# Optimization experiments

Hardware: AMD Instinct MI355X
Metric: run time of the kernel (lower is better)

## Reference

```python
import jax, jax.numpy as jnp
import numpy as np

H = 8  # num_heads
NEG = -1000000.0

def _ln(x, g, b):
    m = jnp.mean(x, axis=-1, keepdims=True)
    v = jnp.var(x, axis=-1, keepdims=True)
    return (x - m) / jnp.sqrt(v + 1e-5) * g + b


def setup_inputs() -> dict:
    key = jax.random.key(0)
    ks = jax.random.split(key, 24)
    B, T, D = 8, 1024, 1024
    Lt, Nt, K, Rt, E = 768, 77, 2, 512, 2048
    s = 0.02
    r = lambda i, shape: s * jax.random.normal(ks[i], shape, jnp.float32)
    return {
        "x": jax.random.normal(ks[0], (B, T, D), jnp.float32),
        "xf": jax.random.normal(ks[1], (B, Nt, Lt), jnp.float32),
        "emb": jax.random.normal(ks[2], (B, E), jnp.float32),
        "src_mask": jnp.ones((B, T, 1), jnp.float32),
        "cond_type": jax.random.randint(ks[3], (B, 1, 1), 0, 100),
        "re_motion": jax.random.normal(ks[4], (B, K, Rt, D), jnp.float32),
        "re_text": jax.random.normal(ks[5], (B, K, 1, D), jnp.float32),
        "re_mask": jnp.ones((B, K, Rt), jnp.float32),
        "ln_g": jnp.ones((D,)), "ln_b": jnp.zeros((D,)),
        "tln_g": jnp.ones((Lt,)), "tln_b": jnp.zeros((Lt,)),
        "rn1_g": jnp.ones((2 * D,)), "rn1_b": jnp.zeros((2 * D,)),
        "rn2_g": jnp.ones((D,)), "rn2_b": jnp.zeros((D,)),
        "Wq": r(6, (D, D)), "bq": jnp.zeros((D,)),
        "Wkt": r(7, (Lt, D)), "bkt": jnp.zeros((D,)),
        "Wvt": r(8, (Lt, D)), "bvt": jnp.zeros((D,)),
        "Wkm": r(9, (D, D)), "bkm": jnp.zeros((D,)),
        "Wvm": r(10, (D, D)), "bvm": jnp.zeros((D,)),
        "Wkr": r(11, (2 * D, D)), "bkr": jnp.zeros((D,)),
        "Wvr": r(12, (D, D)), "bvr": jnp.zeros((D,)),  # zero-init in original; random here for nontrivial math
        "We": r(13, (E, 2 * D)), "be": jnp.zeros((2 * D,)),
        "sln_g": jnp.ones((D,)), "sln_b": jnp.zeros((D,)),
        "Wo": r(14, (D, D)), "bo": jnp.zeros((D,)),  # zero-init in original
    }


def reference(x, xf, emb, src_mask, cond_type, re_motion, re_text, re_mask,
              ln_g, ln_b, tln_g, tln_b, rn1_g, rn1_b, rn2_g, rn2_b,
              Wq, bq, Wkt, bkt, Wvt, bvt, Wkm, bkm, Wvm, bvm,
              Wkr, bkr, Wvr, bvr, We, be, sln_g, sln_b, Wo, bo):
    B, T, D = x.shape
    K, Rt = re_motion.shape[1], re_motion.shape[2]

    norm_x = _ln(x, ln_g, ln_b)
    norm_xf = _ln(xf, tln_g, tln_b)
    query = norm_x @ Wq + bq  # (B,T,D)

    text_ct = (cond_type % 10 > 0).astype(x.dtype)   # (B,1,1)
    retr_ct = (cond_type // 10 > 0).astype(x.dtype)  # (B,1,1)
    re_mask_r = re_mask.reshape(B, -1, 1)            # (B,K*Rt,1)

    # retrieval key features: concat(motion, repeated text) along channels
    re_text_rep = jnp.broadcast_to(re_text, (B, K, Rt, D))
    re_feat_key = jnp.concatenate([re_motion, re_text_rep], axis=-1).reshape(B, -1, 2 * D)

    key_text = norm_xf @ Wkt + bkt + (1.0 - text_ct) * NEG
    key_retr = _ln(re_feat_key, rn1_g, rn1_b) @ Wkr + bkr \
        + (1.0 - retr_ct) * NEG + (1.0 - re_mask_r) * NEG
    key_motion = norm_x @ Wkm + bkm + (1.0 - src_mask) * NEG
    key = jnp.concatenate([key_text, key_retr, key_motion], axis=1)  # (B,N,D)
    N = key.shape[1]

    q = jax.nn.softmax(query.reshape(B, T, H, -1), axis=-1)  # softmax over head dim
    k = jax.nn.softmax(key.reshape(B, N, H, -1), axis=1)     # softmax over tokens

    value_text = (norm_xf @ Wvt + bvt) * text_ct
    value_retr = (_ln(re_motion.reshape(B, -1, D), rn2_g, rn2_b) @ Wvr + bvr) * retr_ct * re_mask_r
    value_motion = (norm_x @ Wvm + bvm) * src_mask
    v = jnp.concatenate([value_text, value_retr, value_motion], axis=1).reshape(B, N, H, -1)

    att = jnp.einsum('bnhd,bnhl->bhdl', k, v)          # (B,H,dh,dh)
    y = jnp.einsum('bthd,bhdl->bthl', q, att).reshape(B, T, D)

    # StylizationBlock: FiLM from time embedding, then zero-init out proj (eval: dropout = id)
    eo = jax.nn.silu(emb) @ We + be                    # (B,2D)
    scale, shift = jnp.split(eo[:, None, :], 2, axis=2)
    h = _ln(y, sln_g, sln_b) * (1.0 + scale) + shift
    h = jax.nn.silu(h) @ Wo + bo
    return x + h
```

## Files before the change

### kernel.cpp

```cpp
#include <hip/hip_runtime.h>
#include <hip/hip_bf16.h>
#include <math.h>

using bf16 = __hip_bfloat16;

typedef short s16x8 __attribute__((ext_vector_type(8)));
typedef short s16x4 __attribute__((ext_vector_type(4)));
typedef float f32x4 __attribute__((ext_vector_type(4)));

constexpr int Bc = 8, Tc = 1024, Dc = 1024, Hc = 8;
constexpr int NTc = 77, LTc = 768, KRc = 1024, Nc = 2125, Ec = 2048;
constexpr float NEGC = -1000000.0f;

constexpr int NP = 2128;
constexpr long SKT = (long)Dc * NP;

constexpr long F_STATS1 = 0;
constexpr long F_STATS2 = F_STATS1 + 16384;
constexpr long F_KEYADD = F_STATS2 + 16384;
constexpr long F_VALMUL = F_KEYADD + 17000;
constexpr long F_SILU   = F_VALMUL + 17000;
constexpr long F_EO     = F_SILU + 16384;
constexpr long F_ATT    = F_EO + 16384;
constexpr long F_END    = F_ATT + 1048576;
constexpr long KT_SZ   = (long)Bc * Dc * NP;
constexpr long B_NORMX = 0;
constexpr long B_Q     = B_NORMX + 8388608;
constexpr long B_KT    = B_Q + 8388608;
constexpr long B_VT    = B_KT + KT_SZ;
constexpr long B_NXF   = B_VT + KT_SZ;
constexpr long B_WQ    = B_NXF + 473088;
constexpr long B_WKM   = B_WQ + 1048576;
constexpr long B_WVM   = B_WKM + 1048576;
constexpr long B_WKT   = B_WVM + 1048576;
constexpr long B_WVT   = B_WKT + 786432;
constexpr long B_WKR   = B_WVT + 786432;
constexpr long B_WVR   = B_WKR + 2097152;
constexpr long B_WO    = B_WVR + 1048576;
constexpr long B_END   = B_WO + 1048576;
constexpr long B_REN2  = B_END;
constexpr long REN2_SZ = 8388608;
constexpr size_t WS_NEED = (size_t)F_END * 4 + (size_t)B_END * 2;
constexpr size_t WS_BIG  = (size_t)F_END * 4 + (size_t)(B_END + REN2_SZ) * 2;

__device__ __forceinline__ float b2f(bf16 v) { return __bfloat162float(v); }
__device__ __forceinline__ bf16 f2b(float v) { return __float2bfloat16(v); }
__device__ __forceinline__ short f2s(float v) {
    bf16 h = __float2bfloat16(v);
    return *reinterpret_cast<short*>(&h);
}
__device__ __forceinline__ float us2f(unsigned short u) {
    bf16 h = *reinterpret_cast<bf16*>(&u);
    return __bfloat162float(h);
}
__device__ __forceinline__ void storef(float* p, float v) { *p = v; }
__device__ __forceinline__ void storef(bf16* p, float v) { *p = __float2bfloat16(v); }

typedef __attribute__((address_space(1))) const unsigned int gu32;
typedef __attribute__((address_space(3))) unsigned int lu32;
__device__ __forceinline__ void gl_lds16(const void* g, void* l) {
    __builtin_amdgcn_global_load_lds((gu32*)g, (lu32*)l, 16, 0, 0);
}

__device__ __forceinline__ float2 block_sum2(float s, float s2) {
    #pragma unroll
    for (int off = 32; off > 0; off >>= 1) {
        s  += __shfl_down(s, off, 64);
        s2 += __shfl_down(s2, off, 64);
    }
    __shared__ float sh[4], sh2[4];
    int w = threadIdx.x >> 6, lane = threadIdx.x & 63;
    if (lane == 0) { sh[w] = s; sh2[w] = s2; }
    __syncthreads();
    s = sh[0] + sh[1] + sh[2] + sh[3];
    s2 = sh2[0] + sh2[1] + sh2[2] + sh2[3];
    return make_float2(s, s2);
}

__device__ __forceinline__ void ln_row_dev(const float* __restrict__ x,
                                           const float* __restrict__ g,
                                           const float* __restrict__ b,
                                           bf16* __restrict__ o, int C) {
    float s = 0.f, s2 = 0.f;
    for (int c = threadIdx.x; c < C; c += 256) { float v = x[c]; s += v; s2 += v * v; }
    float2 r = block_sum2(s, s2);
    float mean = r.x / C;
    float var = r.y / C - mean * mean;
    float inv = rsqrtf(var + 1e-5f);
    for (int c = threadIdx.x; c < C; c += 256)
        o[c] = f2b((x[c] - mean) * inv * g[c] + b[c]);
}

__device__ __forceinline__ s16x4 pack4(float4 v, float mean, float rstd, float4 g, float4 b) {
    s16x4 o;
    o[0] = f2s((v.x - mean) * rstd * g.x + b.x);
    o[1] = f2s((v.y - mean) * rstd * g.y + b.y);
    o[2] = f2s((v.z - mean) * rstd * g.z + b.z);
    o[3] = f2s((v.w - mean) * rstd * g.w + b.w);
    return o;
}

__global__ __launch_bounds__(256) void fused_pre(
    const float* __restrict__ x, const float* __restrict__ ln_g,
    const float* __restrict__ ln_b, bf16* __restrict__ norm_x,
    const float* __restrict__ xf, const float* __restrict__ tln_g,
    const float* __restrict__ tln_b, bf16* __restrict__ nxf,
    const float* __restrict__ motion, const float* __restrict__ text,
    const float* __restrict__ g1, const float* __restrict__ b1,
    const float* __restrict__ g2, const float* __restrict__ b2,
    bf16* __restrict__ ren1, bf16* __restrict__ ren2,
    const int* __restrict__ cond_type, const float* __restrict__ src_mask,
    const float* __restrict__ re_mask,
    float* __restrict__ key_add, float* __restrict__ val_mul,
    bf16* __restrict__ vT) {
    int bid = blockIdx.x;
    if (bid < 8192) {
        long row = bid;
        ln_row_dev(x + row * 1024, ln_g, ln_b, norm_x + row * 1024, 1024);
    } else if (bid < 8808) {
        long row = bid - 8192;
        ln_row_dev(xf + row * 768, tln_g, tln_b, nxf + row * 768, 768);
    } else if (bid < 17000) {
        long row = bid - 8808;
        int c = threadIdx.x * 4;
        const float* mrow = motion + row * 1024;
        const float* trow = text + (row >> 9) * 1024;
        float4 mv = *(const float4*)(mrow + c);
        float4 tv = *(const float4*)(trow + c);
        float sm = mv.x + mv.y + mv.z + mv.w;
        float sm2 = mv.x * mv.x + mv.y * mv.y + mv.z * mv.z + mv.w * mv.w;
        float2 rm = block_sum2(sm, sm2);
        __syncthreads();
        float st = tv.x + tv.y + tv.z + tv.w;
        float st2 = tv.x * tv.x + tv.y * tv.y + tv.z * tv.z + tv.w * tv.w;
        float2 rt = block_sum2(st, st2);
        float mean2 = rm.x / 1024.f;
        float var2 = rm.y / 1024.f - mean2 * mean2;
        float r2 = rsqrtf(var2 + 1e-5f);
        float mean1 = (rm.x + rt.x) / 2048.f;
        float var1 = (rm.y + rt.y) / 2048.f - mean1 * mean1;
        float r1 = rsqrtf(var1 + 1e-5f);
        float4 g1m = *(const float4*)(g1 + c),        b1m = *(const float4*)(b1 + c);
        float4 g1t = *(const float4*)(g1 + 1024 + c), b1t = *(const float4*)(b1 + 1024 + c);
        float4 g2m = *(const float4*)(g2 + c),        b2m = *(const float4*)(b2 + c);
        *(s16x4*)((short*)ren1 + row * 2048 + c)        = pack4(mv, mean1, r1, g1m, b1m);
        *(s16x4*)((short*)ren1 + row * 2048 + 1024 + c) = pack4(tv, mean1, r1, g1t, b1t);
        *(s16x4*)((short*)ren2 + row * 1024 + c)        = pack4(mv, mean2, r2, g2m, b2m);
    } else {
        int b2i = bid - 17000;
        if (b2i < 67) {
            int idx = b2i * 256 + threadIdx.x;
            if (idx >= Bc * Nc) return;
            int b = idx / Nc, n = idx % Nc;
            int ct = cond_type[b];
            float text_ct = ((ct % 10) > 0) ? 1.f : 0.f;
            float retr_ct = ((ct / 10) > 0) ? 1.f : 0.f;
            float add, mul;
            if (n < NTc) {
                add = (1.f - text_ct) * NEGC; mul = text_ct;
            } else if (n < NTc + KRc) {
                float rm = re_mask[b * KRc + (n - NTc)];
                add = (1.f - retr_ct) * NEGC + (1.f - rm) * NEGC;
                mul = retr_ct * rm;
            } else {
                float sm = src_mask[b * Tc + (n - NTc - KRc)];
                add = (1.f - sm) * NEGC; mul = sm;
            }
            key_add[idx] = add;
            val_mul[idx] = mul;
        } else {
            int row = (b2i - 67) * 256 + threadIdx.x;
            if (row >= Bc * Dc) return;
            bf16* p = vT + (long)row * NP + Nc;
            p[0] = f2b(0.f); p[1] = f2b(0.f); p[2] = f2b(0.f);
        }
    }
}

__global__ __launch_bounds__(256) void fused_w(
    const float* __restrict__ Wq,  const float* __restrict__ Wkt,
    const float* __restrict__ Wvt, const float* __restrict__ Wkm,
    const float* __restrict__ Wvm, const float* __restrict__ Wkr,
    const float* __restrict__ Wvr, const float* __restrict__ Wo,
    short* __restrict__ WtQ,  short* __restrict__ WtKT,
    short* __restrict__ WtVT, short* __restrict__ WtKM,
    short* __restrict__ WtVM, short* __restrict__ WtKR,
    short* __restrict__ WtVR, short* __restrict__ WtO,
    const float* __restrict__ emb, const float* __restrict__ We,
    float* __restrict__ part) {
    __shared__ float t[32][33];
    int bid = blockIdx.x;
    if (bid < 8704) {
        int sy = bid >> 5;
        int n0 = (bid & 31) * 32;
        const float* W; short* Wt; int K; int ky;
        if (sy < 32)       { W = Wq;  Wt = WtQ;  K = 1024; ky = sy; }
        else if (sy < 56)  { W = Wkt; Wt = WtKT; K = 768;  ky = sy - 32; }
        else if (sy < 80)  { W = Wvt; Wt = WtVT; K = 768;  ky = sy - 56; }
        else if (sy < 112) { W = Wkm; Wt = WtKM; K = 1024; ky = sy - 80; }
        else if (sy < 144) { W = Wvm; Wt = WtVM; K = 1024; ky = sy - 112; }
        else if (sy < 208) { W = Wkr; Wt = WtKR; K = 2048; ky = sy - 144; }
        else if (sy < 240) { W = Wvr; Wt = WtVR; K = 1024; ky = sy - 208; }
        else               { W = Wo;  Wt = WtO;  K = 1024; ky = sy - 240; }
        int k0 = ky * 32;
        int tx = threadIdx.x & 31, ty = threadIdx.x >> 5;
        #pragma unroll
        for (int i = 0; i < 4; ++i)
            t[ty + i * 8][tx] = W[(long)(k0 + ty + i * 8) * 1024 + n0 + tx];
        __syncthreads();
        #pragma unroll
        for (int i = 0; i < 4; ++i)
            Wt[(long)(n0 + ty + i * 8) * K + k0 + tx] = f2s(t[tx][ty + i * 8]);
    } else {
        int l = bid - 8704;
        int nb = l & 7, ks = l >> 3;
        int n = nb * 256 + threadIdx.x;
        int k0 = ks * 64;
        __shared__ float a_s[8][64];
        for (int idx = threadIdx.x; idx < 512; idx += 256) {
            int b = idx >> 6, kk = idx & 63;
            float v = emb[b * 2048 + k0 + kk];
            a_s[b][kk] = v / (1.f + expf(-v));
        }
        __syncthreads();
        float acc[8] = {};
        for (int kk = 0; kk < 64; ++kk) {
            float w = We[(long)(k0 + kk) * 2048 + n];
            #pragma unroll
            for (int b = 0; b < 8; ++b) acc[b] = fmaf(a_s[b][kk], w, acc[b]);
        }
        #pragma unroll
        for (int b = 0; b < 8; ++b) part[((long)ks * 8 + b) * 2048 + n] = acc[b];
    }
}

constexpr int LDK = 64;

__global__ __launch_bounds__(256) void gemm_mega(
    const short* __restrict__ norm_x, const short* __restrict__ ren1,
    const short* __restrict__ ren2, const short* __restrict__ nxf,
    const short* __restrict__ WtQKVM, const short* __restrict__ WtKR,
    const short* __restrict__ WtVR, const short* __restrict__ WtTXT,
    const float* __restrict__ bq, const float* __restrict__ bkm,
    const float* __restrict__ bvm, const float* __restrict__ bkr,
    const float* __restrict__ bvr,
    const float* __restrict__ bkt, const float* __restrict__ bvt,
    const float* __restrict__ key_add, const float* __restrict__ val_mul,
    bf16* __restrict__ q16, bf16* __restrict__ kT, bf16* __restrict__ vT) {
    int jid = blockIdx.x;
    int sect, tm, tn, K, M, lda, bb = 0;
    const short* A; const short* Bt;
    if (jid < 512) {
        sect = 0;
        int s = (jid & 7) * 64 + (jid >> 3);
        bb = s >> 6; int r = s & 63;
        tm = (r >> 3) * 128; tn = (r & 7) * 128;
        A = ren1 + (long)bb * KRc * 2048; lda = 2048; K = 2048; M = 1024;
        Bt = WtKR;
    } else if (jid < 2048) {
        sect = 1;
        int l = jid - 512;
        int s = (l & 7) * 192 + (l >> 3);
        tn = (s % 24) * 128; tm = (s / 24) * 128;
        A = norm_x; lda = 1024; K = 1024; M = 8192;
        Bt = WtQKVM;
    } else if (jid < 2176) {
        sect = 2;
        int l = jid - 2048;
        bb = l >> 4; tn = (l & 15) * 128; tm = 0;
        A = nxf + (long)bb * NTc * LTc; lda = 768; K = 768; M = 77;
        Bt = WtTXT;
    } else {
        sect = 3;
        int l = jid - 2176;
        int s = (l & 7) * 64 + (l >> 3);
        bb = s >> 6; int r = s & 63;
        tm = (r >> 3) * 128; tn = (r & 7) * 128;
        A = ren2 + (long)bb * KRc * 1024; lda = 1024; K = 1024; M = 1024;
        Bt = WtVR;
    }
    const int ldb = lda;
    const bool swap_ops = !(sect == 1 && tn < 1024);

    __shared__ __align__(16) short As[128 * LDK];
    __shared__ __align__(16) short Bs[128 * LDK];

    int tid = threadIdx.x;
    int lane = tid & 63, wid = tid >> 6;
    int wi = wid >> 1, wj = wid & 1;
    int l16 = lane & 15, quad = lane >> 4;

    f32x4 acc[4][4];
    #pragma unroll
    for (int i = 0; i < 4; ++i)
        #pragma unroll
        for (int j = 0; j < 4; ++j)
            acc[i][j] = (f32x4){0.f, 0.f, 0.f, 0.f};

    auto issue = [&](int k0) {
        #pragma unroll
        for (int p = 0; p < 4; ++p) {
            int e = p * 256 + tid;
            int row = e >> 3, c8 = e & 7;
            int gm = tm + row;
            if (gm >= M) gm = M - 1;
            gl_lds16(A + (long)gm * lda + k0 + c8 * 8, &As[row * LDK + c8 * 8]);
            gl_lds16(Bt + (long)(tn + row) * ldb + k0 + c8 * 8, &Bs[row * LDK + c8 * 8]);
        }
    };

    issue(0);
    int kt = 0;
    while (true) {
        __syncthreads();
        #pragma unroll
        for (int kk = 0; kk < 2; ++kk) {
            s16x8 af[4], bfr[4];
            #pragma unroll
            for (int i = 0; i < 4; ++i)
                af[i] = *(const s16x8*)&As[(wi * 64 + i * 16 + l16) * LDK + kk * 32 + quad * 8];
            #pragma unroll
            for (int j = 0; j < 4; ++j)
                bfr[j] = *(const s16x8*)&Bs[(wj * 64 + j * 16 + l16) * LDK + kk * 32 + quad * 8];
            if (swap_ops) {
                #pragma unroll
                for (int i = 0; i < 4; ++i)
                    #pragma unroll
                    for (int j = 0; j < 4; ++j)
                        acc[i][j] = __builtin_amdgcn_mfma_f32_16x16x32_bf16(bfr[j], af[i], acc[i][j], 0, 0, 0);
            } else {
                #pragma unroll
                for (int i = 0; i < 4; ++i)
                    #pragma unroll
                    for (int j = 0; j < 4; ++j)
                        acc[i][j] = __builtin_amdgcn_mfma_f32_16x16x32_bf16(af[i], bfr[j], acc[i][j], 0, 0, 0);
            }
        }
        int nxt = kt + 64;
        if (nxt >= K) break;
        __syncthreads();
        issue(nxt);
        kt = nxt;
    }

    if (sect == 1 && tn < 1024) {
        #pragma unroll
        for (int i = 0; i < 4; ++i) {
            #pragma unroll
            for (int r = 0; r < 4; ++r) {
                int gm = tm + wi * 64 + i * 16 + quad * 4 + r;
                #pragma unroll
                for (int j = 0; j < 4; ++j) {
                    int gn = tn + wj * 64 + j * 16 + l16;
                    q16[(long)gm * Dc + gn] = f2b(acc[i][j][r] + bq[gn]);
                }
            }
        }
    } else if (sect == 1) {
        int sec = tn >> 10, fn0 = tn & 1023;
        const float* bias = (sec == 1) ? bkm : bvm;
        bf16* C = (sec == 1) ? kT : vT;
        #pragma unroll
        for (int j = 0; j < 4; ++j) {
            #pragma unroll
            for (int r = 0; r < 4; ++r) {
                int feat = fn0 + wj * 64 + j * 16 + quad * 4 + r;
                float bf_ = bias[feat];
                #pragma unroll
                for (int i = 0; i < 4; ++i) {
                    int gm = tm + wi * 64 + i * 16 + l16;
                    int b = gm >> 10, tok = gm & 1023;
                    int mi = b * Nc + NTc + KRc + tok;
                    float v = acc[i][j][r] + bf_;
                    if (sec == 1) v += key_add[mi];
                    else          v *= val_mul[mi];
                    C[(long)b * SKT + (long)feat * NP + NTc + KRc + tok] = f2b(v);
                }
            }
        }
    } else if (sect == 0) {
        const float* rmask = key_add + bb * Nc + NTc;
        bf16* C = kT + (long)bb * SKT + NTc;
        #pragma unroll
        for (int j = 0; j < 4; ++j) {
            #pragma unroll
            for (int r = 0; r < 4; ++r) {
                int feat = tn + wj * 64 + j * 16 + quad * 4 + r;
                float bf_ = bkr[feat];
                #pragma unroll
                for (int i = 0; i < 4; ++i) {
                    int tok = tm + wi * 64 + i * 16 + l16;
                    C[(long)feat * NP + tok] = f2b(acc[i][j][r] + bf_ + rmask[tok]);
                }
            }
        }
    } else if (sect == 3) {
        const float* rmask = val_mul + bb * Nc + NTc;
        bf16* C = vT + (long)bb * SKT + NTc;
        #pragma unroll
        for (int j = 0; j < 4; ++j) {
            #pragma unroll
            for (int r = 0; r < 4; ++r) {
                int feat = tn + wj * 64 + j * 16 + quad * 4 + r;
                float bf_ = bvr[feat];
                #pragma unroll
                for (int i = 0; i < 4; ++i) {
                    int tok = tm + wi * 64 + i * 16 + l16;
                    C[(long)feat * NP + tok] = f2b((acc[i][j][r] + bf_) * rmask[tok]);
                }
            }
        }
    } else {
        int sec = tn >> 10, fn0 = tn & 1023;
        const float* bias = sec ? bvt : bkt;
        const float* rmask = (sec ? val_mul : key_add) + bb * Nc;
        bf16* C = (sec ? vT : kT) + (long)bb * SKT;
        #pragma unroll
        for (int j = 0; j < 4; ++j) {
            #pragma unroll
            for (int r = 0; r < 4; ++r) {
                int feat = fn0 + wj * 64 + j * 16 + quad * 4 + r;
                float bf_ = bias[feat];
                #pragma unroll
                for (int i = 0; i < 4; ++i) {
                    int tok = wi * 64 + i * 16 + l16;
                    if (tok >= NTc) continue;
                    float v = acc[i][j][r] + bf_;
                    if (sec) v *= rmask[tok];
                    else     v += rmask[tok];
                    C[(long)feat * NP + tok] = f2b(v);
                }
            }
        }
    }
}

__global__ __launch_bounds__(256) void gemm_vr(
    const short* __restrict__ ren2, const short* __restrict__ WtVR,
    const float* __restrict__ bvr, const float* __restrict__ val_mul,
    bf16* __restrict__ vT) {
    int s = (blockIdx.x & 7) * 64 + (blockIdx.x >> 3);
    int b = s >> 6; int r = s & 63;
    const int tm = (r >> 3) * 128;
    const int tn = (r & 7) * 128;
    const short* A = ren2 + (long)b * KRc * 1024;
    const float* rmask = val_mul + b * Nc + NTc;
    bf16* C = vT + (long)b * SKT + NTc;

    __shared__ __align__(16) short As[128 * LDK];
    __shared__ __align__(16) short Bs[128 * LDK];

    int tid = threadIdx.x;
    int lane = tid & 63, wid = tid >> 6;
    int wi = wid >> 1, wj = wid & 1;
    int l16 = lane & 15, quad = lane >> 4;

    f32x4 acc[4][4];
    #pragma unroll
    for (int i = 0; i < 4; ++i)
        #pragma unroll
        for (int j = 0; j < 4; ++j)
            acc[i][j] = (f32x4){0.f, 0.f, 0.f, 0.f};

    auto issue = [&](int k0) {
        #pragma unroll
        for (int p = 0; p < 4; ++p) {
            int e = p * 256 + tid;
            int row = e >> 3, c8 = e & 7;
            gl_lds16(A + (long)(tm + row) * 1024 + k0 + c8 * 8, &As[row * LDK + c8 * 8]);
            gl_lds16(WtVR + (long)(tn + row) * 1024 + k0 + c8 * 8, &Bs[row * LDK + c8 * 8]);
        }
    };

    issue(0);
    int kt = 0;
    while (true) {
        __syncthreads();
        #pragma unroll
        for (int kk = 0; kk < 2; ++kk) {
            s16x8 af[4], bfr[4];
            #pragma unroll
            for (int i = 0; i < 4; ++i)
                af[i] = *(const s16x8*)&As[(wi * 64 + i * 16 + l16) * LDK + kk * 32 + quad * 8];
            #pragma unroll
            for (int j = 0; j < 4; ++j)
                bfr[j] = *(const s16x8*)&Bs[(wj * 64 + j * 16 + l16) * LDK + kk * 32 + quad * 8];
            #pragma unroll
            for (int i = 0; i < 4; ++i)
                #pragma unroll
                for (int j = 0; j < 4; ++j)
                    acc[i][j] = __builtin_amdgcn_mfma_f32_16x16x32_bf16(bfr[j], af[i], acc[i][j], 0, 0, 0);
        }
        int nxt = kt + 64;
        if (nxt >= 1024) break;
        __syncthreads();
        issue(nxt);
        kt = nxt;
    }

    #pragma unroll
    for (int j = 0; j < 4; ++j) {
        #pragma unroll
        for (int r2 = 0; r2 < 4; ++r2) {
            int feat = tn + wj * 64 + j * 16 + quad * 4 + r2;
            float bf_ = bvr[feat];
            #pragma unroll
            for (int i = 0; i < 4; ++i) {
                int tok = tm + wi * 64 + i * 16 + l16;
                C[(long)feat * NP + tok] = f2b((acc[i][j][r2] + bf_) * rmask[tok]);
            }
        }
    }
}

__global__ __launch_bounds__(256) void gemm_out(
    const short* __restrict__ A, const short* __restrict__ Bt,
    const float* __restrict__ bias, const float* __restrict__ addC,
    float* __restrict__ C) {
    int s = (blockIdx.x & 7) * 128 + (blockIdx.x >> 3);
    const int tm = (s >> 4) * 128;
    const int tn = (s & 15) * 64;

    __shared__ __align__(16) short As[128 * LDK];
    __shared__ __align__(16) short Bs[64 * LDK];

    int tid = threadIdx.x;
    int lane = tid & 63, wid = tid >> 6;
    int wi = wid >> 1, wj = wid & 1;
    int l16 = lane & 15, quad = lane >> 4;

    f32x4 acc[4][2];
    #pragma unroll
    for (int i = 0; i < 4; ++i)
        #pragma unroll
        for (int j = 0; j < 2; ++j)
            acc[i][j] = (f32x4){0.f, 0.f, 0.f, 0.f};

    auto issue = [&](int k0) {
        #pragma unroll
        for (int p = 0; p < 4; ++p) {
            int e = p * 256 + tid;
            int row = e >> 3, c8 = e & 7;
            gl_lds16(A + (long)(tm + row) * 1024 + k0 + c8 * 8, &As[row * LDK + c8 * 8]);
        }
        #pragma unroll
        for (int p = 0; p < 2; ++p) {
            int e = p * 256 + tid;
            int row = e >> 3, c8 = e & 7;
            gl_lds16(Bt + (long)(tn + row) * 1024 + k0 + c8 * 8, &Bs[row * LDK + c8 * 8]);
        }
    };

    issue(0);
    int kt = 0;
    while (true) {
        __syncthreads();
        #pragma unroll
        for (int kk = 0; kk < 2; ++kk) {
            s16x8 af[4], bfr[2];
            #pragma unroll
            for (int i = 0; i < 4; ++i)
                af[i] = *(const s16x8*)&As[(wi * 64 + i * 16 + l16) * LDK + kk * 32 + quad * 8];
            #pragma unroll
            for (int j = 0; j < 2; ++j)
                bfr[j] = *(const s16x8*)&Bs[(wj * 32 + j * 16 + l16) * LDK + kk * 32 + quad * 8];
            #pragma unroll
            for (int i = 0; i < 4; ++i)
                #pragma unroll
                for (int j = 0; j < 2; ++j)
                    acc[i][j] = __builtin_amdgcn_mfma_f32_16x16x32_bf16(af[i], bfr[j], acc[i][j], 0, 0, 0);
        }
        int nxt = kt + 64;
        if (nxt >= 1024) break;
        __syncthreads();
        issue(nxt);
        kt = nxt;
    }

    #pragma unroll
    for (int i = 0; i < 4; ++i) {
        #pragma unroll
        for (int r = 0; r < 4; ++r) {
            int gm = tm + wi * 64 + i * 16 + quad * 4 + r;
            #pragma unroll
            for (int j = 0; j < 2; ++j) {
                int gn = tn + wj * 32 + j * 16 + l16;
                C[(long)gm * 1024 + gn] = acc[i][j][r] + bias[gn] + addC[(long)gm * 1024 + gn];
            }
        }
    }
}

__global__ __launch_bounds__(256) void fused_sm(
    bf16* __restrict__ q, const bf16* __restrict__ kT,
    float* __restrict__ cs_m, float* __restrict__ cs_inv,
    const float* __restrict__ part, const float* __restrict__ be,
    float* __restrict__ eo) {
    int bid = blockIdx.x;
    int lane = threadIdx.x & 63;
    if (bid < 16384) {
        long row = (long)bid * 4 + (threadIdx.x >> 6);
        bf16* p = q + row * 128 + lane * 2;
        float v0 = b2f(p[0]), v1 = b2f(p[1]);
        float mx = fmaxf(v0, v1);
        #pragma unroll
        for (int off = 32; off > 0; off >>= 1) mx = fmaxf(mx, __shfl_xor(mx, off, 64));
        float e0 = expf(v0 - mx), e1 = expf(v1 - mx);
        float s = e0 + e1;
        #pragma unroll
        for (int off = 32; off > 0; off >>= 1) s += __shfl_xor(s, off, 64);
        float inv = 1.f / s;
        p[0] = f2b(e0 * inv);
        p[1] = f2b(e1 * inv);
    } else if (bid < 18432) {
        int row = (bid - 16384) * 4 + (threadIdx.x >> 6);
        const s16x8* p8 = (const s16x8*)(kT + (long)row * NP);
        float m = -3.0e38f;
        for (int c = lane; c < NP / 8; c += 64) {
            s16x8 raw = p8[c];
            int n0 = c * 8;
            #pragma unroll
            for (int j = 0; j < 8; ++j)
                if (n0 + j < Nc) m = fmaxf(m, us2f((unsigned short)raw[j]));
        }
        #pragma unroll
        for (int off = 32; off > 0; off >>= 1) m = fmaxf(m, __shfl_xor(m, off, 64));
        float s = 0.f;
        for (int c = lane; c < NP / 8; c += 64) {
            s16x8 raw = p8[c];
            int n0 = c * 8;
            #pragma unroll
            for (int j = 0; j < 8; ++j)
                if (n0 + j < Nc) s += __expf(us2f((unsigned short)raw[j]) - m);
        }
        #pragma unroll
        for (int off = 32; off > 0; off >>= 1) s += __shfl_xor(s, off, 64);
        if (lane == 0) { cs_m[row] = m; cs_inv[row] = 1.f / s; }
    } else {
        int idx = (bid - 18432) * 256 + threadIdx.x;
        int n = idx & 2047, b = idx >> 11;
        float s = be[n];
        #pragma unroll 8
        for (int ks = 0; ks < 32; ++ks) s += part[((long)ks * 8 + b) * 2048 + n];
        eo[idx] = s;
    }
}

constexpr int ATT_SPLIT = 8;
__global__ __launch_bounds__(256) void att_gemm(const bf16* __restrict__ kTb,
                                                const bf16* __restrict__ vTb,
                                                const float* __restrict__ cs_m,
                                                float* __restrict__ att_part) {
    int bh = blockIdx.x;
    int split = blockIdx.y;
    int b = bh >> 3, h = bh & 7;
    const short* A  = (const short*)kTb + ((long)b * 1024 + h * 128) * NP;
    const short* Bt = (const short*)vTb + ((long)b * 1024 + h * 128) * NP;
    float* ap = att_part + ((long)split * 64 + bh) * 16384;

    __shared__ __align__(16) short As[128 * LDK];
    __shared__ __align__(16) short Bs[128 * LDK];
    __shared__ float ms[128];

    int tid = threadIdx.x;
    if (tid < 128) ms[tid] = cs_m[(long)b * 1024 + h * 128 + tid];

    int lane = tid & 63, wid = tid >> 6;
    int wi = wid >> 1, wj = wid & 1;
    int l16 = lane & 15, quad = lane >> 4;

    f32x4 acc[4][4];
    #pragma unroll
    for (int i = 0; i < 4; ++i)
        #pragma unroll
        for (int j = 0; j < 4; ++j)
            acc[i][j] = (f32x4){0.f, 0.f, 0.f, 0.f};

    uint4 pa[4];
    auto computeA = [&](int k0) {
        #pragma unroll
        for (int p = 0; p < 4; ++p) {
            int e = p * 256 + tid;
            int row = e >> 3, c8 = e & 7;
            int n0 = k0 + c8 * 8;
            union { short s[8]; uint4 u; } pk;
            if (n0 >= Nc) {
                pk.u = (uint4){0u, 0u, 0u, 0u};
            } else {
                float m = ms[row];
                s16x8 raw = *(const s16x8*)(A + (long)row * NP + n0);
                #pragma unroll
                for (int j = 0; j < 8; ++j) {
                    float v = (n0 + j < Nc) ? __expf(us2f((unsigned short)raw[j]) - m) : 0.f;
                    pk.s[j] = f2s(v);
                }
            }
            pa[p] = pk.u;
        }
    };
    auto issueB = [&](int k0) {
        #pragma unroll
        for (int p = 0; p < 4; ++p) {
            int e = p * 256 + tid;
            int row = e >> 3, c8 = e & 7;
            int n0 = k0 + c8 * 8;
            if (n0 > NP - 8) n0 = NP - 8;
            gl_lds16(Bt + (long)row * NP + n0, &Bs[row * LDK + c8 * 8]);
        }
    };
    auto storeA = [&]() {
        #pragma unroll
        for (int p = 0; p < 4; ++p) {
            int e = p * 256 + tid;
            int row = e >> 3, c8 = e & 7;
            *(uint4*)&As[row * LDK + c8 * 8] = pa[p];
        }
    };

    int st = (split < 2) ? split * 5 : 10 + (split - 2) * 4;
    int cnt = (split < 2) ? 5 : 4;
    int kt = st * 64;
    int kend = kt + cnt * 64;

    __syncthreads();
    issueB(kt);
    computeA(kt);
    storeA();
    while (true) {
        __syncthreads();
        #pragma unroll
        for (int kk = 0; kk < 2; ++kk) {
            s16x8 af[4], bfr[4];
            #pragma unroll
            for (int i = 0; i < 4; ++i)
                af[i] = *(const s16x8*)&As[(wi * 64 + i * 16 + l16) * LDK + kk * 32 + quad * 8];
            #pragma unroll
            for (int j = 0; j < 4; ++j)
                bfr[j] = *(const s16x8*)&Bs[(wj * 64 + j * 16 + l16) * LDK + kk * 32 + quad * 8];
            #pragma unroll
            for (int i = 0; i < 4; ++i)
                #pragma unroll
                for (int j = 0; j < 4; ++j)
                    acc[i][j] = __builtin_amdgcn_mfma_f32_16x16x32_bf16(bfr[j], af[i], acc[i][j], 0, 0, 0);
        }
        int nxt = kt + 64;
        if (nxt >= kend) break;
        computeA(nxt);
        __syncthreads();
        issueB(nxt);
        storeA();
        kt = nxt;
    }

    #pragma unroll
    for (int j = 0; j < 4; ++j) {
        #pragma unroll
        for (int r = 0; r < 4; ++r) {
            int l = wj * 64 + j * 16 + quad * 4 + r;
            #pragma unroll
            for (int i = 0; i < 4; ++i) {
                int d = wi * 64 + i * 16 + l16;
                ap[l * 128 + d] = acc[i][j][r];
            }
        }
    }
}

__global__ __launch_bounds__(256) void reduce_att_t(const float* __restrict__ att_part,
                                                    const float* __restrict__ cs_inv,
                                                    bf16* __restrict__ attT) {
    long idx = (long)blockIdx.x * 256 + threadIdx.x;
    if (idx >= (long)64 * 16384) return;
    float s = 0.f;
    #pragma unroll
    for (int sp = 0; sp < ATT_SPLIT; ++sp) s += att_part[(long)sp * 64 * 16384 + idx];
    int bh = (int)(idx >> 14);
    int d = (int)(idx & 127);
    int b = bh >> 3, h = bh & 7;
    attT[idx] = f2b(s * cs_inv[b * Dc + h * 128 + d]);
}

__global__ __launch_bounds__(256) void y_gemm(const bf16* __restrict__ q,
                                              const bf16* __restrict__ attT,
                                              bf16* __restrict__ y) {
    int bh = blockIdx.y;
    int b = bh >> 3, h = bh & 7;
    const short* A  = (const short*)q + (long)b * Tc * Dc + h * 128;
    const short* Bt = (const short*)attT + (long)bh * 16384;
    bf16* yb = y + (long)b * Tc * Dc + h * 128;
    int tm = blockIdx.x * 128;

    __shared__ __align__(16) short As[128 * 128];
    __shared__ __align__(16) short Bs[128 * 128];
    int tid = threadIdx.x;
    #pragma unroll
    for (int p = 0; p < 8; ++p) {
        int e = p * 256 + tid;
        int row = e >> 4, c8 = e & 15;
        gl_lds16(A + (long)(tm + row) * Dc + c8 * 8, &As[row * 128 + c8 * 8]);
        gl_lds16(Bt + row * 128 + c8 * 8, &Bs[row * 128 + c8 * 8]);
    }
    int lane = tid & 63, wid = tid >> 6;
    int wi = wid >> 1, wj = wid & 1;
    int l16 = lane & 15, quad = lane >> 4;
    f32x4 acc[4][4];
    #pragma unroll
    for (int i = 0; i < 4; ++i)
        #pragma unroll
        for (int j = 0; j < 4; ++j)
            acc[i][j] = (f32x4){0.f, 0.f, 0.f, 0.f};
    __syncthreads();
    #pragma unroll
    for (int kk = 0; kk < 4; ++kk) {
        s16x8 af[4], bfr[4];
        #pragma unroll
        for (int i = 0; i < 4; ++i)
            af[i] = *(const s16x8*)&As[(wi * 64 + i * 16 + l16) * 128 + kk * 32 + quad * 8];
        #pragma unroll
        for (int j = 0; j < 4; ++j)
            bfr[j] = *(const s16x8*)&Bs[(wj * 64 + j * 16 + l16) * 128 + kk * 32 + quad * 8];
        #pragma unroll
        for (int i = 0; i < 4; ++i)
            #pragma unroll
            for (int j = 0; j < 4; ++j)
                acc[i][j] = __builtin_amdgcn_mfma_f32_16x16x32_bf16(af[i], bfr[j], acc[i][j], 0, 0, 0);
    }
    #pragma unroll
    for (int i = 0; i < 4; ++i) {
        #pragma unroll
        for (int r = 0; r < 4; ++r) {
            int gm = tm + wi * 64 + i * 16 + quad * 4 + r;
            #pragma unroll
            for (int j = 0; j < 4; ++j) {
                int gn = wj * 64 + j * 16 + l16;
                yb[(long)gm * Dc + gn] = f2b(acc[i][j][r]);
            }
        }
    }
}

__global__ __launch_bounds__(256) void film_kernel(const bf16* __restrict__ y,
                                                   const float* __restrict__ eo,
                                                   const float* __restrict__ g,
                                                   const float* __restrict__ bta,
                                                   bf16* __restrict__ s) {
    long row = blockIdx.x;
    int b = (int)(row >> 10);
    const bf16* yr = y + row * Dc;
    float sum = 0.f, sum2 = 0.f;
    for (int c = threadIdx.x; c < Dc; c += 256) { float v = b2f(yr[c]); sum += v; sum2 += v * v; }
    float2 r = block_sum2(sum, sum2);
    float mean = r.x / Dc;
    float var = r.y / Dc - mean * mean;
    float inv = rsqrtf(var + 1e-5f);
    const float* sc = eo + (long)b * 2048;
    const float* sf = sc + 1024;
    bf16* so = s + row * Dc;
    for (int c = threadIdx.x; c < Dc; c += 256) {
        float v = (b2f(yr[c]) - mean) * inv * g[c] + bta[c];
        v = v * (1.f + sc[c]) + sf[c];
        so[c] = f2b(v / (1.f + expf(-v)));
    }
}

extern "C" void kernel_launch(void* const* d_in, const int* in_sizes, int n_in,
                              void* d_out, int out_size, void* d_ws, size_t ws_size,
                              hipStream_t stream) {
    if (ws_size < WS_NEED) return;
    const bool big = ws_size >= WS_BIG;

    const float* x         = (const float*)d_in[0];
    const float* xf        = (const float*)d_in[1];
    const float* emb       = (const float*)d_in[2];
    const float* src_mask  = (const float*)d_in[3];
    const int*   cond_type = (const int*)d_in[4];
    const float* re_motion = (const float*)d_in[5];
    const float* re_text   = (const float*)d_in[6];
    const float* re_mask   = (const float*)d_in[7];
    const float* ln_g  = (const float*)d_in[8];
    const float* ln_b  = (const float*)d_in[9];
    const float* tln_g = (const float*)d_in[10];
    const float* tln_b = (const float*)d_in[11];
    const float* rn1_g = (const float*)d_in[12];
    const float* rn1_b = (const float*)d_in[13];
    const float* rn2_g = (const float*)d_in[14];
    const float* rn2_b = (const float*)d_in[15];
    const float* Wq  = (const float*)d_in[16];
    const float* bq  = (const float*)d_in[17];
    const float* Wkt = (const float*)d_in[18];
    const float* bkt = (const float*)d_in[19];
    const float* Wvt = (const float*)d_in[20];
    const float* bvt = (const float*)d_in[21];
    const float* Wkm = (const float*)d_in[22];
    const float* bkm = (const float*)d_in[23];
    const float* Wvm = (const float*)d_in[24];
    const float* bvm = (const float*)d_in[25];
    const float* Wkr = (const float*)d_in[26];
    const float* bkr = (const float*)d_in[27];
    const float* Wvr = (const float*)d_in[28];
    const float* bvr = (const float*)d_in[29];
    const float* We  = (const float*)d_in[30];
    const float* be  = (const float*)d_in[31];
    const float* sln_g = (const float*)d_in[32];
    const float* sln_b = (const float*)d_in[33];
    const float* Wo  = (const float*)d_in[34];
    const float* bo  = (const float*)d_in[35];

    float* ws = (float*)d_ws;
    float* key_add  = ws + F_KEYADD;
    float* val_mul  = ws + F_VALMUL;
    float* cs_m     = ws + F_SILU;
    float* cs_inv   = cs_m + Bc * Dc;
    float* eo       = ws + F_EO;
    bf16*  attT     = (bf16*)(ws + F_ATT);
    float* eo_part  = ws + F_ATT + 524288;
    bf16* wb = (bf16*)(ws + F_END);
    bf16* norm_x16 = wb + B_NORMX;
    bf16* q16      = wb + B_Q;
    bf16* kT16     = wb + B_KT;
    bf16* vT16     = wb + B_VT;
    bf16* nxf16    = wb + B_NXF;
    short* WtQ  = (short*)(wb + B_WQ);
    short* WtKM = (short*)(wb + B_WKM);
    short* WtVM = (short*)(wb + B_WVM);
    short* WtKT = (short*)(wb + B_WKT);
    short* WtVT = (short*)(wb + B_WVT);
    short* WtKR = (short*)(wb + B_WKR);
    short* WtVR = (short*)(wb + B_WVR);
    short* WtO  = (short*)(wb + B_WO);
    bf16* y16 = wb + B_NORMX;
    bf16* s16 = q16;
    bf16* ren1 = (bf16*)d_out;
    float* att_part = (float*)d_out;
    bf16* ren2 = big ? (wb + B_REN2) : q16;

    float* out = (float*)d_out;

    fused_pre<<<dim3(17099), dim3(256), 0, stream>>>(
        x, ln_g, ln_b, norm_x16, xf, tln_g, tln_b, nxf16,
        re_motion, re_text, rn1_g, rn1_b, rn2_g, rn2_b, ren1, ren2,
        cond_type, src_mask, re_mask, key_add, val_mul, vT16);

    fused_w<<<dim3(8960), dim3(256), 0, stream>>>(
        Wq, Wkt, Wvt, Wkm, Wvm, Wkr, Wvr, Wo,
        WtQ, WtKT, WtVT, WtKM, WtVM, WtKR, WtVR, WtO,
        emb, We, eo_part);

    if (!big)
        gemm_vr<<<dim3(512), dim3(256), 0, stream>>>(
            (const short*)ren2, WtVR, bvr, val_mul, vT16);

    gemm_mega<<<dim3(big ? 2688 : 2176), dim3(256), 0, stream>>>(
        (const short*)norm_x16, (const short*)ren1, (const short*)ren2,
        (const short*)nxf16, WtQ, WtKR, WtVR, WtKT,
        bq, bkm, bvm, bkr, bvr, bkt, bvt,
        key_add, val_mul, q16, kT16, vT16);

    fused_sm<<<dim3(18496), dim3(256), 0, stream>>>(
        q16, kT16, cs_m, cs_inv, eo_part, be, eo);

    att_gemm<<<dim3(Bc * Hc, ATT_SPLIT), dim3(256), 0, stream>>>(kT16, vT16, cs_m, att_part);
    reduce_att_t<<<dim3((64 * 16384 + 255) / 256), dim3(256), 0, stream>>>(att_part, cs_inv, attT);

    y_gemm<<<dim3(Tc / 128, Bc * Hc), dim3(256), 0, stream>>>(q16, attT, y16);

    film_kernel<<<dim3(Bc * Tc), dim3(256), 0, stream>>>(y16, eo, sln_g, sln_b, s16);

    gemm_out<<<dim3(1024), dim3(256), 0, stream>>>(
        (const short*)s16, WtO, bo, x, out);
}
```

Before: 570.6 us.

## Double-buffer LDS in GEMM kernels and vectorize layernorm/FiLM row kernels

The three GEMM kernels now use two LDS buffers, so the global-to-LDS load for the next K tile is issued before computing the current one, overlapping memory latency with MFMA work. The layernorm and FiLM row kernels switch from strided scalar loops to one float4 (or 4×bf16) load per thread with a single pass over registers. Double buffering doubles shared memory per block, which may lower occupancy.

Result: no change. 561.6 us (-1.6%).

```diff
diff --git a/kernel.cpp b/kernel.cpp
--- a/kernel.cpp
+++ b/kernel.cpp
@@ -77,18 +77,29 @@
     return make_float2(s, s2);
 }
 
-__device__ __forceinline__ void ln_row_dev(const float* __restrict__ x,
+__device__ __forceinline__ void ln_row_vec(const float* __restrict__ x,
                                            const float* __restrict__ g,
                                            const float* __restrict__ b,
                                            bf16* __restrict__ o, int C) {
-    float s = 0.f, s2 = 0.f;
-    for (int c = threadIdx.x; c < C; c += 256) { float v = x[c]; s += v; s2 += v * v; }
+    int c = threadIdx.x * 4;
+    bool act = c < C;
+    float4 v = make_float4(0.f, 0.f, 0.f, 0.f);
+    if (act) v = *(const float4*)(x + c);
+    float s = v.x + v.y + v.z + v.w;
+    float s2 = v.x * v.x + v.y * v.y + v.z * v.z + v.w * v.w;
     float2 r = block_sum2(s, s2);
     float mean = r.x / C;
     float var = r.y / C - mean * mean;
     float inv = rsqrtf(var + 1e-5f);
-    for (int c = threadIdx.x; c < C; c += 256)
-        o[c] = f2b((x[c] - mean) * inv * g[c] + b[c]);
+    if (act) {
+        float4 gv = *(const float4*)(g + c), bv = *(const float4*)(b + c);
+        s16x4 ov;
+        ov[0] = f2s((v.x - mean) * inv * gv.x + bv.x);
+        ov[1] = f2s((v.y - mean) * inv * gv.y + bv.y);
+        ov[2] = f2s((v.z - mean) * inv * gv.z + bv.z);
+        ov[3] = f2s((v.w - mean) * inv * gv.w + bv.w);
+        *(s16x4*)((short*)o + c) = ov;
+    }
 }
 
 __device__ __forceinline__ s16x4 pack4(float4 v, float mean, float rstd, float4 g, float4 b) {
@@ -116,10 +127,10 @@
     int bid = blockIdx.x;
     if (bid < 8192) {
         long row = bid;
-        ln_row_dev(x + row * 1024, ln_g, ln_b, norm_x + row * 1024, 1024);
+        ln_row_vec(x + row * 1024, ln_g, ln_b, norm_x + row * 1024, 1024);
     } else if (bid < 8808) {
         long row = bid - 8192;
-        ln_row_dev(xf + row * 768, tln_g, tln_b, nxf + row * 768, 768);
+        ln_row_vec(xf + row * 768, tln_g, tln_b, nxf + row * 768, 768);
     } else if (bid < 17000) {
         long row = bid - 8808;
         int c = threadIdx.x * 4;
@@ -282,8 +293,8 @@
     const int ldb = lda;
     const bool swap_ops = !(sect == 1 && tn < 1024);
 
-    __shared__ __align__(16) short As[128 * LDK];
-    __shared__ __align__(16) short Bs[128 * LDK];
+    __shared__ __align__(16) short As[2][128 * LDK];
+    __shared__ __align__(16) short Bs[2][128 * LDK];
 
     int tid = threadIdx.x;
     int lane = tid & 63, wid = tid >> 6;
@@ -297,31 +308,29 @@
         for (int j = 0; j < 4; ++j)
             acc[i][j] = (f32x4){0.f, 0.f, 0.f, 0.f};
 
-    auto issue = [&](int k0) {
+    auto issue = [&](int k0, int buf) {
         #pragma unroll
         for (int p = 0; p < 4; ++p) {
             int e = p * 256 + tid;
             int row = e >> 3, c8 = e & 7;
             int gm = tm + row;
             if (gm >= M) gm = M - 1;
-            gl_lds16(A + (long)gm * lda + k0 + c8 * 8, &As[row * LDK + c8 * 8]);
-            gl_lds16(Bt + (long)(tn + row) * ldb + k0 + c8 * 8, &Bs[row * LDK + c8 * 8]);
+            gl_lds16(A + (long)gm * lda + k0 + c8 * 8, &As[buf][row * LDK + c8 * 8]);
+            gl_lds16(Bt + (long)(tn + row) * ldb + k0 + c8 * 8, &Bs[buf][row * LDK + c8 * 8]);
         }
     };
-
-    issue(0);
-    int kt = 0;
-    while (true) {
-        __syncthreads();
+    auto compute = [&](int buf) {
+        const short* as = As[buf];
+        const short* bs = Bs[buf];
         #pragma unroll
         for (int kk = 0; kk < 2; ++kk) {
             s16x8 af[4], bfr[4];
             #pragma unroll
             for (int i = 0; i < 4; ++i)
-                af[i] = *(const s16x8*)&As[(wi * 64 + i * 16 + l16) * LDK + kk * 32 + quad * 8];
+                af[i] = *(const s16x8*)&as[(wi * 64 + i * 16 + l16) * LDK + kk * 32 + quad * 8];
             #pragma unroll
             for (int j = 0; j < 4; ++j)
-                bfr[j] = *(const s16x8*)&Bs[(wj * 64 + j * 16 + l16) * LDK + kk * 32 + quad * 8];
+                bfr[j] = *(const s16x8*)&bs[(wj * 64 + j * 16 + l16) * LDK + kk * 32 + quad * 8];
             if (swap_ops) {
                 #pragma unroll
                 for (int i = 0; i < 4; ++i)
@@ -336,10 +345,18 @@
                         acc[i][j] = __builtin_amdgcn_mfma_f32_16x16x32_bf16(af[i], bfr[j], acc[i][j], 0, 0, 0);
             }
         }
+    };
+
+    issue(0, 0);
+    __syncthreads();
+    int cur = 0, kt = 0;
+    while (true) {
         int nxt = kt + 64;
+        if (nxt < K) issue(nxt, cur ^ 1);
+        compute(cur);
         if (nxt >= K) break;
         __syncthreads();
-        issue(nxt);
+        cur ^= 1;
         kt = nxt;
     }
 
@@ -447,8 +464,8 @@
     const float* rmask = val_mul + b * Nc + NTc;
     bf16* C = vT + (long)b * SKT + NTc;
 
-    __shared__ __align__(16) short As[128 * LDK];
-    __shared__ __align__(16) short Bs[128 * LDK];
+    __shared__ __align__(16) short As[2][128 * LDK];
+    __shared__ __align__(16) short Bs[2][128 * LDK];
 
     int tid = threadIdx.x;
     int lane = tid & 63, wid = tid >> 6;
@@ -462,39 +479,45 @@
         for (int j = 0; j < 4; ++j)
             acc[i][j] = (f32x4){0.f, 0.f, 0.f, 0.f};
 
-    auto issue = [&](int k0) {
+    auto issue = [&](int k0, int buf) {
         #pragma unroll
         for (int p = 0; p < 4; ++p) {
             int e = p * 256 + tid;
             int row = e >> 3, c8 = e & 7;
-            gl_lds16(A + (long)(tm + row) * 1024 + k0 + c8 * 8, &As[row * LDK + c8 * 8]);
-            gl_lds16(WtVR + (long)(tn + row) * 1024 + k0 + c8 * 8, &Bs[row * LDK + c8 * 8]);
+            gl_lds16(A + (long)(tm + row) * 1024 + k0 + c8 * 8, &As[buf][row * LDK + c8 * 8]);
+            gl_lds16(WtVR + (long)(tn + row) * 1024 + k0 + c8 * 8, &Bs[buf][row * LDK + c8 * 8]);
         }
     };
-
-    issue(0);
-    int kt = 0;
-    while (true) {
-        __syncthreads();
+    auto compute = [&](int buf) {
+        const short* as = As[buf];
+        const short* bs = Bs[buf];
         #pragma unroll
         for (int kk = 0; kk < 2; ++kk) {
             s16x8 af[4], bfr[4];
             #pragma unroll
             for (int i = 0; i < 4; ++i)
-                af[i] = *(const s16x8*)&As[(wi * 64 + i * 16 + l16) * LDK + kk * 32 + quad * 8];
+                af[i] = *(const s16x8*)&as[(wi * 64 + i * 16 + l16) * LDK + kk * 32 + quad * 8];
             #pragma unroll
             for (int j = 0; j < 4; ++j)
-                bfr[j] = *(const s16x8*)&Bs[(wj * 64 + j * 16 + l16) * LDK + kk * 32 + quad * 8];
+                bfr[j] = *(const s16x8*)&bs[(wj * 64 + j * 16 + l16) * LDK + kk * 32 + quad * 8];
             #pragma unroll
             for (int i = 0; i < 4; ++i)
                 #pragma unroll
                 for (int j = 0; j < 4; ++j)
                     acc[i][j] = __builtin_amdgcn_mfma_f32_16x16x32_bf16(bfr[j], af[i], acc[i][j], 0, 0, 0);
         }
+    };
+
+    issue(0, 0);
+    __syncthreads();
+    int cur = 0, kt = 0;
+    while (true) {
         int nxt = kt + 64;
+        if (nxt < 1024) issue(nxt, cur ^ 1);
+        compute(cur);
         if (nxt >= 1024) break;
         __syncthreads();
-        issue(nxt);
+        cur ^= 1;
         kt = nxt;
     }
 
@@ -521,8 +544,8 @@
     const int tm = (s >> 4) * 128;
     const int tn = (s & 15) * 64;
 
-    __shared__ __align__(16) short As[128 * LDK];
-    __shared__ __align__(16) short Bs[64 * LDK];
+    __shared__ __align__(16) short As[2][128 * LDK];
+    __shared__ __align__(16) short Bs[2][64 * LDK];
 
     int tid = threadIdx.x;
     int lane = tid & 63, wid = tid >> 6;
@@ -536,44 +559,50 @@
         for (int j = 0; j < 2; ++j)
             acc[i][j] = (f32x4){0.f, 0.f, 0.f, 0.f};
 
-    auto issue = [&](int k0) {
+    auto issue = [&](int k0, int buf) {
         #pragma unroll
         for (int p = 0; p < 4; ++p) {
             int e = p * 256 + tid;
             int row = e >> 3, c8 = e & 7;
-            gl_lds16(A + (long)(tm + row) * 1024 + k0 + c8 * 8, &As[row * LDK + c8 * 8]);
+            gl_lds16(A + (long)(tm + row) * 1024 + k0 + c8 * 8, &As[buf][row * LDK + c8 * 8]);
         }
         #pragma unroll
         for (int p = 0; p < 2; ++p) {
             int e = p * 256 + tid;
             int row = e >> 3, c8 = e & 7;
-            gl_lds16(Bt + (long)(tn + row) * 1024 + k0 + c8 * 8, &Bs[row * LDK + c8 * 8]);
+            gl_lds16(Bt + (long)(tn + row) * 1024 + k0 + c8 * 8, &Bs[buf][row * LDK + c8 * 8]);
         }
     };
-
-    issue(0);
-    int kt = 0;
-    while (true) {
-        __syncthreads();
+    auto compute = [&](int buf) {
+        const short* as = As[buf];
+        const short* bs = Bs[buf];
         #pragma unroll
         for (int kk = 0; kk < 2; ++kk) {
             s16x8 af[4], bfr[2];
             #pragma unroll
             for (int i = 0; i < 4; ++i)
-                af[i] = *(const s16x8*)&As[(wi * 64 + i * 16 + l16) * LDK + kk * 32 + quad * 8];
+                af[i] = *(const s16x8*)&as[(wi * 64 + i * 16 + l16) * LDK + kk * 32 + quad * 8];
             #pragma unroll
             for (int j = 0; j < 2; ++j)
-                bfr[j] = *(const s16x8*)&Bs[(wj * 32 + j * 16 + l16) * LDK + kk * 32 + quad * 8];
+                bfr[j] = *(const s16x8*)&bs[(wj * 32 + j * 16 + l16) * LDK + kk * 32 + quad * 8];
             #pragma unroll
             for (int i = 0; i < 4; ++i)
                 #pragma unroll
                 for (int j = 0; j < 2; ++j)
                     acc[i][j] = __builtin_amdgcn_mfma_f32_16x16x32_bf16(af[i], bfr[j], acc[i][j], 0, 0, 0);
         }
+    };
+
+    issue(0, 0);
+    __syncthreads();
+    int cur = 0, kt = 0;
+    while (true) {
         int nxt = kt + 64;
+        if (nxt < 1024) issue(nxt, cur ^ 1);
+        compute(cur);
         if (nxt >= 1024) break;
         __syncthreads();
-        issue(nxt);
+        cur ^= 1;
         kt = nxt;
     }
 
@@ -846,21 +875,33 @@
                                                    bf16* __restrict__ s) {
     long row = blockIdx.x;
     int b = (int)(row >> 10);
-    const bf16* yr = y + row * Dc;
-    float sum = 0.f, sum2 = 0.f;
-    for (int c = threadIdx.x; c < Dc; c += 256) { float v = b2f(yr[c]); sum += v; sum2 += v * v; }
+    int c = threadIdx.x * 4;
+    s16x4 raw = *(const s16x4*)((const short*)(y + row * Dc) + c);
+    float v0 = us2f((unsigned short)raw[0]);
+    float v1 = us2f((unsigned short)raw[1]);
+    float v2 = us2f((unsigned short)raw[2]);
+    float v3 = us2f((unsigned short)raw[3]);
+    float sum = v0 + v1 + v2 + v3;
+    float sum2 = v0 * v0 + v1 * v1 + v2 * v2 + v3 * v3;
     float2 r = block_sum2(sum, sum2);
     float mean = r.x / Dc;
     float var = r.y / Dc - mean * mean;
     float inv = rsqrtf(var + 1e-5f);
     const float* sc = eo + (long)b * 2048;
     const float* sf = sc + 1024;
-    bf16* so = s + row * Dc;
-    for (int c = threadIdx.x; c < Dc; c += 256) {
-        float v = (b2f(yr[c]) - mean) * inv * g[c] + bta[c];
-        v = v * (1.f + sc[c]) + sf[c];
-        so[c] = f2b(v / (1.f + expf(-v)));
-    }
+    float4 gv = *(const float4*)(g + c), bv = *(const float4*)(bta + c);
+    float4 scv = *(const float4*)(sc + c), sfv = *(const float4*)(sf + c);
+    auto fl = [&](float v, float gg, float bb, float ss, float ff) {
+        float t = (v - mean) * inv * gg + bb;
+        t = t * (1.f + ss) + ff;
+        return t / (1.f + expf(-t));
+    };
+    s16x4 o;
+    o[0] = f2s(fl(v0, gv.x, bv.x, scv.x, sfv.x));
+    o[1] = f2s(fl(v1, gv.y, bv.y, scv.y, sfv.y));
+    o[2] = f2s(fl(v2, gv.z, bv.z, scv.z, sfv.z));
+    o[3] = f2s(fl(v3, gv.w, bv.w, scv.w, sfv.w));
+    *(s16x4*)((short*)(s + row * Dc) + c) = o;
 }
 
 extern "C" void kernel_launch(void* const* d_in, const int* in_sizes, int n_in,
```
